# Kernel tuning notes

Hardware: AMD Instinct MI355X
Metric: run time of the kernel (lower is better)

## Reference

```python
import math
import jax, jax.numpy as jnp
import numpy as np

PAD_IDX = 1
SEP_ID = 4
STARTPOS = 1025
BSZ, SEQ_LEN, EMBED_DIM = 32, 4096, 1024


def _build_table(num_cons, dim, padding_idx, startpos):
    # Sinusoidal table, identical to ConsPosiEmb.get_embedding (dim is even here).
    half = dim // 2
    freqs = jnp.exp(jnp.arange(half, dtype=jnp.float32) * -(math.log(10000.0) / (half - 1)))
    ang = jnp.arange(startpos, startpos + num_cons, dtype=jnp.float32)[:, None] * freqs[None, :]
    tab = jnp.concatenate([jnp.sin(ang), jnp.cos(ang)], axis=1)  # [num_cons, dim]
    return tab.at[padding_idx].set(0.0)


def setup_inputs() -> dict:
    key = jax.random.key(0)
    tokens = jax.random.randint(key, (BSZ, SEQ_LEN), 0, 1000, dtype=jnp.int64)
    # forward rebuilds weights with max_pos = padding_idx + 1 + seq_len rows
    num_cons = PAD_IDX + 1 + SEQ_LEN
    weights = _build_table(num_cons, EMBED_DIM, PAD_IDX, STARTPOS)
    return {"input": tokens, "weights": weights}


def _positions(tokens):
    # Vectorized equivalent of the Python double loop in get_positions:
    #   padding -> 1 (and everything after the first padding stays 1: `break`),
    #   sep     -> 2,
    #   other   -> previous + 1 (starts at 2 via the ones-initialized wrap-around).
    L = tokens.shape[1]
    valid = jnp.cumprod((tokens != PAD_IDX).astype(jnp.int32), axis=1).astype(bool)
    j = jnp.arange(L, dtype=jnp.int32)
    # running max of last sep index (virtual sep at index 0 reproduces the start-at-2 behavior)
    sep_j = jnp.where(tokens == SEP_ID, j, 0)
    last_sep = jax.lax.associative_scan(jnp.maximum, sep_j, axis=1)
    pos = j - last_sep + 2  # sep itself -> 2, then 3, 4, ...
    return jnp.where(valid, pos, 1)


def reference(input, weights):
    pos = _positions(input)                # [bsz, seq_len] int32, in [1, seq_len+1]
    return jnp.take(weights, pos, axis=0)  # [bsz, seq_len, embed_dim]
```

## Files before the change

kernel.cpp:

```cpp
#include <hip/hip_runtime.h>
#include <climits>

#define PAD_IDX 1
#define SEP_ID 4

__global__ __launch_bounds__(256) void pos_kernel(const int* __restrict__ tokens,
                                                  int* __restrict__ pos,
                                                  int seq_len) {
    const int row  = blockIdx.x;
    const int t    = threadIdx.x;
    const int CH   = seq_len >> 8;
    const int rbase = row * seq_len;
    const int ebase = t * CH;

    int toks[16];
    const int4* tp = (const int4*)(tokens + rbase + ebase);
    #pragma unroll
    for (int k = 0; k < 4; ++k) {
        int4 v = tp[k];
        toks[k*4+0] = v.x; toks[k*4+1] = v.y; toks[k*4+2] = v.z; toks[k*4+3] = v.w;
    }

    int localMaxSep = 0;
    int localMinPad = INT_MAX;
    #pragma unroll
    for (int k = 0; k < 16; ++k) {
        int j = ebase + k;
        if (toks[k] == SEP_ID)  localMaxSep = max(localMaxSep, j);
        if (toks[k] == PAD_IDX) localMinPad = min(localMinPad, j);
    }

    __shared__ int sMax[256];
    __shared__ int sMin[256];
    sMax[t] = localMaxSep;
    sMin[t] = localMinPad;
    __syncthreads();
    for (int off = 1; off < 256; off <<= 1) {
        int vM = 0, vN = INT_MAX;
        if (t >= off) { vM = sMax[t - off]; vN = sMin[t - off]; }
        __syncthreads();
        sMax[t] = max(sMax[t], vM);
        sMin[t] = min(sMin[t], vN);
        __syncthreads();
    }
    int lastSep  = (t > 0) ? sMax[t - 1] : 0;
    int firstPad = (t > 0) ? sMin[t - 1] : INT_MAX;

    int outv[16];
    #pragma unroll
    for (int k = 0; k < 16; ++k) {
        int j   = ebase + k;
        int tok = toks[k];
        if (tok == PAD_IDX) firstPad = min(firstPad, j);
        if (tok == SEP_ID)  lastSep  = max(lastSep, j);
        outv[k] = (firstPad <= j) ? 1 : (j - lastSep + 2);
    }
    int4* op = (int4*)(pos + rbase + ebase);
    #pragma unroll
    for (int k = 0; k < 4; ++k) {
        op[k] = make_int4(outv[k*4+0], outv[k*4+1], outv[k*4+2], outv[k*4+3]);
    }
}

__global__ __launch_bounds__(256) void gather_kernel(const float4* __restrict__ w,
                                                     const int* __restrict__ pos,
                                                     float4* __restrict__ out) {
    const int row = blockIdx.x;
    const int d   = threadIdx.x;
    const int p   = pos[row];
    out[(size_t)row * 256 + d] = w[(size_t)p * 256 + d];
}

extern "C" void kernel_launch(void* const* d_in, const int* in_sizes, int n_in,
                              void* d_out, int out_size, void* d_ws, size_t ws_size,
                              hipStream_t stream) {
    const int*   tokens  = (const int*)d_in[0];
    const float* weights = (const float*)d_in[1];
    float*       out     = (float*)d_out;

    const int seq_len = 4096;
    const int rows    = in_sizes[0] / seq_len;

    int* pos = (int*)d_ws;

    pos_kernel<<<rows, 256, 0, stream>>>(tokens, pos, seq_len);
    gather_kernel<<<rows * seq_len, 256, 0, stream>>>((const float4*)weights, pos,
                                                      (float4*)out);
}
```

Baseline: 529.6 us.

## Fuse position scan into gather kernel with 64 rows per block

Merges the position-computation and gather kernels into one launch. Each block recomputes the full per-row prefix scan over 4096 tokens, keeps the 64 positions for its own segment in shared memory, then copies 64 embedding rows instead of one row per block. This removes the second launch, the workspace round trip for positions, and the one-row-per-block launch overhead. In exchange each row's token scan is repeated 64 times.

```diff
diff --git a/kernel.cpp b/kernel.cpp
--- a/kernel.cpp
+++ b/kernel.cpp
@@ -4,14 +4,17 @@
 #define PAD_IDX 1
 #define SEP_ID 4
 
-__global__ __launch_bounds__(256) void pos_kernel(const int* __restrict__ tokens,
-                                                  int* __restrict__ pos,
-                                                  int seq_len) {
-    const int row  = blockIdx.x;
-    const int t    = threadIdx.x;
-    const int CH   = seq_len >> 8;
-    const int rbase = row * seq_len;
-    const int ebase = t * CH;
+typedef float floatx4 __attribute__((ext_vector_type(4)));
+
+__global__ __launch_bounds__(256) void fused_kernel(const int* __restrict__ tokens,
+                                                    const floatx4* __restrict__ w,
+                                                    floatx4* __restrict__ out,
+                                                    int seq_len) {
+    const int b   = blockIdx.x >> 6;
+    const int seg = blockIdx.x & 63;
+    const int t   = threadIdx.x;
+    const int rbase = b * seq_len;
+    const int ebase = t * 16;
 
     int toks[16];
     const int4* tp = (const int4*)(tokens + rbase + ebase);
@@ -32,6 +35,7 @@
 
     __shared__ int sMax[256];
     __shared__ int sMin[256];
+    __shared__ int posBuf[64];
     sMax[t] = localMaxSep;
     sMin[t] = localMinPad;
     __syncthreads();
@@ -43,32 +47,37 @@
         sMin[t] = min(sMin[t], vN);
         __syncthreads();
     }
+
     int lastSep  = (t > 0) ? sMax[t - 1] : 0;
     int firstPad = (t > 0) ? sMin[t - 1] : INT_MAX;
+    if ((t >> 2) == seg) {
+        #pragma unroll
+        for (int k = 0; k < 16; ++k) {
+            int j   = ebase + k;
+            int tok = toks[k];
+            if (tok == PAD_IDX) firstPad = min(firstPad, j);
+            if (tok == SEP_ID)  lastSep  = max(lastSep, j);
+            posBuf[(t & 3) * 16 + k] = (firstPad <= j) ? 1 : (j - lastSep + 2);
+        }
+    }
+    __syncthreads();
 
-    int outv[16];
-    #pragma unroll
-    for (int k = 0; k < 16; ++k) {
-        int j   = ebase + k;
-        int tok = toks[k];
-        if (tok == PAD_IDX) firstPad = min(firstPad, j);
-        if (tok == SEP_ID)  lastSep  = max(lastSep, j);
-        outv[k] = (firstPad <= j) ? 1 : (j - lastSep + 2);
+    const size_t outRow0 = (size_t)blockIdx.x * 64;
+    #pragma unroll 2
+    for (int r = 0; r < 64; r += 4) {
+        const int p0 = posBuf[r + 0];
+        const int p1 = posBuf[r + 1];
+        const int p2 = posBuf[r + 2];
+        const int p3 = posBuf[r + 3];
+        floatx4 v0 = w[(size_t)p0 * 256 + t];
+        floatx4 v1 = w[(size_t)p1 * 256 + t];
+        floatx4 v2 = w[(size_t)p2 * 256 + t];
+        floatx4 v3 = w[(size_t)p3 * 256 + t];
+        out[(outRow0 + r + 0) * 256 + t] = v0;
+        out[(outRow0 + r + 1) * 256 + t] = v1;
+        out[(outRow0 + r + 2) * 256 + t] = v2;
+        out[(outRow0 + r + 3) * 256 + t] = v3;
     }
-    int4* op = (int4*)(pos + rbase + ebase);
-    #pragma unroll
-    for (int k = 0; k < 4; ++k) {
-        op[k] = make_int4(outv[k*4+0], outv[k*4+1], outv[k*4+2], outv[k*4+3]);
-    }
-}
-
-__global__ __launch_bounds__(256) void gather_kernel(const float4* __restrict__ w,
-                                                     const int* __restrict__ pos,
-                                                     float4* __restrict__ out) {
-    const int row = blockIdx.x;
-    const int d   = threadIdx.x;
-    const int p   = pos[row];
-    out[(size_t)row * 256 + d] = w[(size_t)p * 256 + d];
 }
 
 extern "C" void kernel_launch(void* const* d_in, const int* in_sizes, int n_in,
@@ -81,9 +90,6 @@
     const int seq_len = 4096;
     const int rows    = in_sizes[0] / seq_len;
 
-    int* pos = (int*)d_ws;
-
-    pos_kernel<<<rows, 256, 0, stream>>>(tokens, pos, seq_len);
-    gather_kernel<<<rows * seq_len, 256, 0, stream>>>((const float4*)weights, pos,
-                                                      (float4*)out);
+    fused_kernel<<<rows * 64, 256, 0, stream>>>(tokens, (const floatx4*)weights,
+                                                (floatx4*)out, seq_len);
 }
```

New measurement: 547.6 us. 1.03x slower.
